# Performance work log

Hardware: AMD Instinct MI355X
Metric: run time of the kernel (lower is better)

## Reference

```python
import jax, jax.numpy as jnp
import numpy as np

B, NMEL, TF = 64, 80, 1000      # batch, mel channels, mel frames
NDEC, TENC = 1000, 200          # alignment dims
NSPK, NAUG = 100, 10
K_ALIGN = 0.4
LAMB = 0.0005


def setup_inputs() -> dict:
    key = jax.random.key(0)
    ks = jax.random.split(key, 10)
    return {
        "mel_out": jax.random.normal(ks[0], (B, NMEL, TF), jnp.float32),
        "mel_out_postnet": jax.random.normal(ks[1], (B, NMEL, TF), jnp.float32),
        "gate_out": jax.random.normal(ks[2], (B, TF), jnp.float32),
        "alignment": jax.random.uniform(ks[3], (B, NDEC, TENC), jnp.float32),
        "speaker_out": jax.random.normal(ks[4], (B, NSPK), jnp.float32),
        "augment_out": jax.random.normal(ks[5], (B, NAUG), jnp.float32),
        "mel_target": jax.random.normal(ks[6], (B, NMEL, TF), jnp.float32),
        "gate_target": (jax.random.uniform(ks[7], (B, TF)) > 0.9).astype(jnp.float32),
        "speaker_target": jax.random.uniform(ks[8], (B, NSPK), jnp.float32),
        "aug_target": jax.random.uniform(ks[9], (B, NAUG), jnp.float32),
        "step": 1000,
    }


def _ce(logits, labels):
    # mean cross-entropy with integer labels
    logp = jax.nn.log_softmax(logits, axis=-1)
    return -jnp.mean(jnp.take_along_axis(logp, labels[:, None], axis=1))


def reference(mel_out, mel_out_postnet, gate_out, alignment, speaker_out,
              augment_out, mel_target, gate_target, speaker_target, aug_target, step):
    # MSE losses (mean reduction)
    mel_loss = jnp.mean((mel_out - mel_target) ** 2) + \
               jnp.mean((mel_out_postnet - mel_target) ** 2)
    # BCE with logits (mean): softplus(x) - x*y
    gate_loss = jnp.mean(jax.nn.softplus(gate_out) - gate_out * gate_target)
    # cross-entropy against argmax of one-hot-ish targets
    speaker_loss = _ce(speaker_out, jnp.argmax(speaker_target, axis=1))
    augment_loss = _ce(augment_out, jnp.argmax(aug_target, axis=1))
    tmp_loss = mel_loss + gate_loss
    # vectorized alignment penalty matrix g[n,t] = 1 - exp(-((n/N - t/T)^2)/k)
    N, T = alignment.shape[1], alignment.shape[2]
    n = jnp.arange(N, dtype=jnp.float32) / N
    t = jnp.arange(T, dtype=jnp.float32) / T
    g = 1.0 - jnp.exp(-((n[:, None] - t[None, :]) ** 2) / K_ALIGN)
    alignment_loss = jnp.abs(jnp.sum(alignment * g[None])) * LAMB
    total_loss = 10.0 * tmp_loss + 0.1 * (speaker_loss + augment_loss) + alignment_loss
    return (total_loss, tmp_loss, speaker_loss, augment_loss, alignment_loss)
```

## Files before the change

kernel.cpp:

```cpp
#include <hip/hip_runtime.h>
#include <hip/hip_bf16.h>

#define BATCH   64
#define NMEL    80
#define TFRAME  1000
#define NDEC    1000
#define TENC    200
#define NSPK    100
#define NAUG    10

#define N_MEL   (BATCH * NMEL * TFRAME)
#define N_GATE  (BATCH * TFRAME)
#define N_ALIGN (BATCH * NDEC * TENC)

#define U_MEL   (N_MEL / 4)
#define U_GATE  (N_GATE / 4)
#define U_ALIGN (N_ALIGN / 4)
#define U_MG    (U_MEL + U_GATE)
#define U_TOTAL (U_MG + U_ALIGN)

#define MAIN_BLOCKS 2048
#define BLOCK 256

#define WS_MEL   0
#define WS_GATE  16
#define WS_ALIGN 32
#define WS_SPK   48
#define WS_AUG   64

__device__ __forceinline__ float waveReduceSum(float v) {
#pragma unroll
    for (int o = 32; o > 0; o >>= 1) v += __shfl_down(v, o, 64);
    return v;
}

__device__ __forceinline__ void fatomic_add(float* p, float v) {
    unsafeAtomicAdd(p, v);
}

__global__ __launch_bounds__(BLOCK) void tacotron2_loss_reduce(
    const float* __restrict__ mel_out,
    const float* __restrict__ mel_post,
    const float* __restrict__ gate_out,
    const float* __restrict__ align,
    const float* __restrict__ spk_out,
    const float* __restrict__ aug_out,
    const float* __restrict__ mel_tgt,
    const float* __restrict__ gate_tgt,
    const float* __restrict__ spk_tgt,
    const float* __restrict__ aug_tgt,
    float* __restrict__ ws)
{
    float mel_s = 0.f, gate_s = 0.f, align_s = 0.f;
    const int bid = blockIdx.x;

    if (bid < MAIN_BLOCKS) {
        const int nthreads = MAIN_BLOCKS * BLOCK;
        const int tid = bid * BLOCK + threadIdx.x;
        for (int u = tid; u < U_TOTAL; u += nthreads) {
            if (u < U_MEL) {
                float4 a = ((const float4*)mel_out)[u];
                float4 p = ((const float4*)mel_post)[u];
                float4 t = ((const float4*)mel_tgt)[u];
                float d;
                d = a.x - t.x; mel_s = fmaf(d, d, mel_s);
                d = a.y - t.y; mel_s = fmaf(d, d, mel_s);
                d = a.z - t.z; mel_s = fmaf(d, d, mel_s);
                d = a.w - t.w; mel_s = fmaf(d, d, mel_s);
                d = p.x - t.x; mel_s = fmaf(d, d, mel_s);
                d = p.y - t.y; mel_s = fmaf(d, d, mel_s);
                d = p.z - t.z; mel_s = fmaf(d, d, mel_s);
                d = p.w - t.w; mel_s = fmaf(d, d, mel_s);
            } else if (u < U_MG) {
                int v = u - U_MEL;
                float4 x = ((const float4*)gate_out)[v];
                float4 y = ((const float4*)gate_tgt)[v];
                float fx[4] = {x.x, x.y, x.z, x.w};
                float fy[4] = {y.x, y.y, y.z, y.w};
#pragma unroll
                for (int j = 0; j < 4; j++) {
                    float xx = fx[j];
                    float sp = fmaxf(xx, 0.f) + log1pf(__expf(-fabsf(xx)));
                    gate_s += sp - xx * fy[j];
                }
            } else {
                int v = u - U_MG;
                float4 a = ((const float4*)align)[v];
                float fa[4] = {a.x, a.y, a.z, a.w};
                int e = v * 4;
                int t0 = e % TENC;
                int n = (e / TENC) % NDEC;
                float nf = (float)n * (1.0f / (float)NDEC);
#pragma unroll
                for (int j = 0; j < 4; j++) {
                    float tf_ = (float)(t0 + j) * (1.0f / (float)TENC);
                    float d = nf - tf_;
                    float g = 1.0f - __expf(d * d * -2.5f);
                    align_s = fmaf(fa[j], g, align_s);
                }
            }
        }
    } else {
        const int t = threadIdx.x;
        if (t < 64) {
            const int r = t;
            const float* row = spk_out + r * NSPK;
            float mx = -1e30f;
            for (int c = 0; c < NSPK; c++) mx = fmaxf(mx, row[c]);
            float se = 0.f;
            for (int c = 0; c < NSPK; c++) se += __expf(row[c] - mx);
            const float* trow = spk_tgt + r * NSPK;
            float tm = -1e30f; int lab = 0;
            for (int c = 0; c < NSPK; c++) {
                float v = trow[c];
                if (v > tm) { tm = v; lab = c; }
            }
            float loss = -(row[lab] - mx - __logf(se));
            loss = waveReduceSum(loss);
            if (t == 0) fatomic_add(&ws[WS_SPK], loss);
        } else if (t < 128) {
            const int r = t - 64;
            const float* row = aug_out + r * NAUG;
            float mx = -1e30f;
            for (int c = 0; c < NAUG; c++) mx = fmaxf(mx, row[c]);
            float se = 0.f;
            for (int c = 0; c < NAUG; c++) se += __expf(row[c] - mx);
            const float* trow = aug_tgt + r * NAUG;
            float tm = -1e30f; int lab = 0;
            for (int c = 0; c < NAUG; c++) {
                float v = trow[c];
                if (v > tm) { tm = v; lab = c; }
            }
            float loss = -(row[lab] - mx - __logf(se));
            loss = waveReduceSum(loss);
            if (t == 64) fatomic_add(&ws[WS_AUG], loss);
        }
    }

    __shared__ float smem[12];
    const int lane = threadIdx.x & 63;
    const int wid = threadIdx.x >> 6;
    mel_s = waveReduceSum(mel_s);
    gate_s = waveReduceSum(gate_s);
    align_s = waveReduceSum(align_s);
    if (lane == 0) {
        smem[wid * 3 + 0] = mel_s;
        smem[wid * 3 + 1] = gate_s;
        smem[wid * 3 + 2] = align_s;
    }
    __syncthreads();

    if (threadIdx.x == 0) {
        float m = 0.f, g = 0.f, al = 0.f;
#pragma unroll
        for (int w = 0; w < 4; w++) {
            m += smem[w * 3 + 0];
            g += smem[w * 3 + 1];
            al += smem[w * 3 + 2];
        }
        fatomic_add(&ws[WS_MEL], m);
        fatomic_add(&ws[WS_GATE], g);
        fatomic_add(&ws[WS_ALIGN], al);
    }
}

__global__ __launch_bounds__(64) void tacotron2_loss_finalize(
    const float* __restrict__ ws, float* __restrict__ out)
{
    if (threadIdx.x == 0) {
        float mel_sum   = __hip_atomic_load(&ws[WS_MEL],   __ATOMIC_RELAXED, __HIP_MEMORY_SCOPE_AGENT);
        float gate_sum  = __hip_atomic_load(&ws[WS_GATE],  __ATOMIC_RELAXED, __HIP_MEMORY_SCOPE_AGENT);
        float align_sum = __hip_atomic_load(&ws[WS_ALIGN], __ATOMIC_RELAXED, __HIP_MEMORY_SCOPE_AGENT);
        float spk_sum   = __hip_atomic_load(&ws[WS_SPK],   __ATOMIC_RELAXED, __HIP_MEMORY_SCOPE_AGENT);
        float aug_sum   = __hip_atomic_load(&ws[WS_AUG],   __ATOMIC_RELAXED, __HIP_MEMORY_SCOPE_AGENT);

        float mel_loss  = mel_sum  * (1.0f / (float)N_MEL);
        float gate_loss = gate_sum * (1.0f / (float)N_GATE);
        float spk_loss  = spk_sum  * (1.0f / (float)BATCH);
        float aug_loss  = aug_sum  * (1.0f / (float)BATCH);
        float align_loss = fabsf(align_sum) * 0.0005f;
        float tmp = mel_loss + gate_loss;
        float total = 10.0f * tmp + 0.1f * (spk_loss + aug_loss) + align_loss;

        out[0] = total;
        out[1] = tmp;
        out[2] = spk_loss;
        out[3] = aug_loss;
        out[4] = align_loss;
    }
}

extern "C" void kernel_launch(void* const* d_in, const int* in_sizes, int n_in,
                              void* d_out, int out_size, void* d_ws, size_t ws_size,
                              hipStream_t stream) {
    const float* mel_out  = (const float*)d_in[0];
    const float* mel_post = (const float*)d_in[1];
    const float* gate_out = (const float*)d_in[2];
    const float* align    = (const float*)d_in[3];
    const float* spk_out  = (const float*)d_in[4];
    const float* aug_out  = (const float*)d_in[5];
    const float* mel_tgt  = (const float*)d_in[6];
    const float* gate_tgt = (const float*)d_in[7];
    const float* spk_tgt  = (const float*)d_in[8];
    const float* aug_tgt  = (const float*)d_in[9];

    float* ws = (float*)d_ws;
    float* out = (float*)d_out;

    hipMemsetAsync(d_ws, 0, 80 * sizeof(float), stream);

    tacotron2_loss_reduce<<<dim3(MAIN_BLOCKS + 1), dim3(BLOCK), 0, stream>>>(
        mel_out, mel_post, gate_out, align, spk_out, aug_out,
        mel_tgt, gate_tgt, spk_tgt, aug_tgt, ws);

    tacotron2_loss_finalize<<<dim3(1), dim3(64), 0, stream>>>(ws, out);
}
```

Baseline: 178.6 us.

## Replace grid-stride loop with per-segment block assignment and batched loads

Drops the grid-stride loop with its per-element branching across mel, gate and alignment. Each block now owns a fixed contiguous chunk of exactly one segment, so the grid is sized to the data (mel 2500 blocks, alignment 3125, gate 16, plus one cross-entropy block). Each thread issues several independent float4 loads up front to raise memory-level parallelism. In exchange there are many more blocks and many more atomics to three global accumulators, and the index math is hardcoded to the problem sizes.

Result: slower. 200.7 us (+12.3%).

```diff
diff --git a/kernel.cpp b/kernel.cpp
--- a/kernel.cpp
+++ b/kernel.cpp
@@ -16,11 +16,17 @@
 #define U_MEL   (N_MEL / 4)
 #define U_GATE  (N_GATE / 4)
 #define U_ALIGN (N_ALIGN / 4)
-#define U_MG    (U_MEL + U_GATE)
-#define U_TOTAL (U_MG + U_ALIGN)
-
-#define MAIN_BLOCKS 2048
+
 #define BLOCK 256
+
+#define MEL_NB   2500
+#define ALIGN_NB 3125
+#define GATE_NB  16
+#define MEL_B0   0
+#define ALIGN_B0 (MEL_B0 + MEL_NB)
+#define GATE_B0  (ALIGN_B0 + ALIGN_NB)
+#define CE_B     (GATE_B0 + GATE_NB)
+#define GRID     (CE_B + 1)
 
 #define WS_MEL   0
 #define WS_GATE  16
@@ -36,6 +42,18 @@
 
 __device__ __forceinline__ void fatomic_add(float* p, float v) {
     unsafeAtomicAdd(p, v);
+}
+
+__device__ __forceinline__ void blockReduceAtomic(float v, float* target) {
+    __shared__ float smem[4];
+    const int lane = threadIdx.x & 63;
+    const int wid = threadIdx.x >> 6;
+    v = waveReduceSum(v);
+    if (lane == 0) smem[wid] = v;
+    __syncthreads();
+    if (threadIdx.x == 0) {
+        fatomic_add(target, smem[0] + smem[1] + smem[2] + smem[3]);
+    }
 }
 
 __global__ __launch_bounds__(BLOCK) void tacotron2_loss_reduce(
@@ -51,57 +69,86 @@
     const float* __restrict__ aug_tgt,
     float* __restrict__ ws)
 {
-    float mel_s = 0.f, gate_s = 0.f, align_s = 0.f;
     const int bid = blockIdx.x;
-
-    if (bid < MAIN_BLOCKS) {
-        const int nthreads = MAIN_BLOCKS * BLOCK;
-        const int tid = bid * BLOCK + threadIdx.x;
-        for (int u = tid; u < U_TOTAL; u += nthreads) {
-            if (u < U_MEL) {
-                float4 a = ((const float4*)mel_out)[u];
-                float4 p = ((const float4*)mel_post)[u];
-                float4 t = ((const float4*)mel_tgt)[u];
-                float d;
-                d = a.x - t.x; mel_s = fmaf(d, d, mel_s);
-                d = a.y - t.y; mel_s = fmaf(d, d, mel_s);
-                d = a.z - t.z; mel_s = fmaf(d, d, mel_s);
-                d = a.w - t.w; mel_s = fmaf(d, d, mel_s);
-                d = p.x - t.x; mel_s = fmaf(d, d, mel_s);
-                d = p.y - t.y; mel_s = fmaf(d, d, mel_s);
-                d = p.z - t.z; mel_s = fmaf(d, d, mel_s);
-                d = p.w - t.w; mel_s = fmaf(d, d, mel_s);
-            } else if (u < U_MG) {
-                int v = u - U_MEL;
-                float4 x = ((const float4*)gate_out)[v];
-                float4 y = ((const float4*)gate_tgt)[v];
+    const int t = threadIdx.x;
+
+    if (bid < ALIGN_B0) {
+        const int base = bid * 512 + t;
+        const float4* ao = (const float4*)mel_out;
+        const float4* po = (const float4*)mel_post;
+        const float4* to = (const float4*)mel_tgt;
+        float4 a0 = ao[base], a1 = ao[base + 256];
+        float4 p0 = po[base], p1 = po[base + 256];
+        float4 t0 = to[base], t1 = to[base + 256];
+        float s = 0.f, d;
+        d = a0.x - t0.x; s = fmaf(d, d, s);
+        d = a0.y - t0.y; s = fmaf(d, d, s);
+        d = a0.z - t0.z; s = fmaf(d, d, s);
+        d = a0.w - t0.w; s = fmaf(d, d, s);
+        d = p0.x - t0.x; s = fmaf(d, d, s);
+        d = p0.y - t0.y; s = fmaf(d, d, s);
+        d = p0.z - t0.z; s = fmaf(d, d, s);
+        d = p0.w - t0.w; s = fmaf(d, d, s);
+        d = a1.x - t1.x; s = fmaf(d, d, s);
+        d = a1.y - t1.y; s = fmaf(d, d, s);
+        d = a1.z - t1.z; s = fmaf(d, d, s);
+        d = a1.w - t1.w; s = fmaf(d, d, s);
+        d = p1.x - t1.x; s = fmaf(d, d, s);
+        d = p1.y - t1.y; s = fmaf(d, d, s);
+        d = p1.z - t1.z; s = fmaf(d, d, s);
+        d = p1.w - t1.w; s = fmaf(d, d, s);
+        blockReduceAtomic(s, &ws[WS_MEL]);
+    } else if (bid < GATE_B0) {
+        const int b = bid - ALIGN_B0;
+        const int base = b * 1024 + t;
+        const float4* av = (const float4*)align;
+        float4 A0 = av[base];
+        float4 A1 = av[base + 256];
+        float4 A2 = av[base + 512];
+        float4 A3 = av[base + 768];
+        float s = 0.f;
+        float4 regs[4] = {A0, A1, A2, A3};
+#pragma unroll
+        for (int k = 0; k < 4; k++) {
+            const int u = base + 256 * k;
+            const int q = u / 50;
+            const int r = u - q * 50;
+            const float nf = (float)(q % NDEC) * (1.0f / (float)NDEC);
+            const float tb = (float)(4 * r) * (1.0f / (float)TENC);
+            const float fa[4] = {regs[k].x, regs[k].y, regs[k].z, regs[k].w};
+#pragma unroll
+            for (int j = 0; j < 4; j++) {
+                float tf_ = tb + (float)j * (1.0f / (float)TENC);
+                float d = nf - tf_;
+                float g = 1.0f - __expf(d * d * -2.5f);
+                s = fmaf(fa[j], g, s);
+            }
+        }
+        blockReduceAtomic(s, &ws[WS_ALIGN]);
+    } else if (bid < CE_B) {
+        const int b = bid - GATE_B0;
+        const int base = b * 1024 + t;
+        const float4* xo = (const float4*)gate_out;
+        const float4* yo = (const float4*)gate_tgt;
+        float s = 0.f;
+#pragma unroll
+        for (int k = 0; k < 4; k++) {
+            const int u = base + 256 * k;
+            if (u < U_GATE) {
+                float4 x = xo[u];
+                float4 y = yo[u];
                 float fx[4] = {x.x, x.y, x.z, x.w};
                 float fy[4] = {y.x, y.y, y.z, y.w};
 #pragma unroll
                 for (int j = 0; j < 4; j++) {
                     float xx = fx[j];
                     float sp = fmaxf(xx, 0.f) + log1pf(__expf(-fabsf(xx)));
-                    gate_s += sp - xx * fy[j];
+                    s += sp - xx * fy[j];
                 }
-            } else {
-                int v = u - U_MG;
-                float4 a = ((const float4*)align)[v];
-                float fa[4] = {a.x, a.y, a.z, a.w};
-                int e = v * 4;
-                int t0 = e % TENC;
-                int n = (e / TENC) % NDEC;
-                float nf = (float)n * (1.0f / (float)NDEC);
-#pragma unroll
-                for (int j = 0; j < 4; j++) {
-                    float tf_ = (float)(t0 + j) * (1.0f / (float)TENC);
-                    float d = nf - tf_;
-                    float g = 1.0f - __expf(d * d * -2.5f);
-                    align_s = fmaf(fa[j], g, align_s);
-                }
             }
         }
+        blockReduceAtomic(s, &ws[WS_GATE]);
     } else {
-        const int t = threadIdx.x;
         if (t < 64) {
             const int r = t;
             const float* row = spk_out + r * NSPK;
@@ -136,32 +183,6 @@
             if (t == 64) fatomic_add(&ws[WS_AUG], loss);
         }
     }
-
-    __shared__ float smem[12];
-    const int lane = threadIdx.x & 63;
-    const int wid = threadIdx.x >> 6;
-    mel_s = waveReduceSum(mel_s);
-    gate_s = waveReduceSum(gate_s);
-    align_s = waveReduceSum(align_s);
-    if (lane == 0) {
-        smem[wid * 3 + 0] = mel_s;
-        smem[wid * 3 + 1] = gate_s;
-        smem[wid * 3 + 2] = align_s;
-    }
-    __syncthreads();
-
-    if (threadIdx.x == 0) {
-        float m = 0.f, g = 0.f, al = 0.f;
-#pragma unroll
-        for (int w = 0; w < 4; w++) {
-            m += smem[w * 3 + 0];
-            g += smem[w * 3 + 1];
-            al += smem[w * 3 + 2];
-        }
-        fatomic_add(&ws[WS_MEL], m);
-        fatomic_add(&ws[WS_GATE], g);
-        fatomic_add(&ws[WS_ALIGN], al);
-    }
 }
 
 __global__ __launch_bounds__(64) void tacotron2_loss_finalize(
@@ -209,7 +230,7 @@
 
     hipMemsetAsync(d_ws, 0, 80 * sizeof(float), stream);
 
-    tacotron2_loss_reduce<<<dim3(MAIN_BLOCKS + 1), dim3(BLOCK), 0, stream>>>(
+    tacotron2_loss_reduce<<<dim3(GRID), dim3(BLOCK), 0, stream>>>(
         mel_out, mel_post, gate_out, align, spk_out, aug_out,
         mel_tgt, gate_tgt, spk_tgt, aug_tgt, ws);
 
```
